# Kernel optimization log

Hardware: AMD Instinct MI355X
Metric: run time of the kernel (lower is better)

## Reference

```python
import jax, jax.numpy as jnp
import numpy as np

NTOKENS = 8192
TOPK = 2
HIDDEN = 4096
NUM_GROUPS = 2
M_FULL = NTOKENS * TOPK


def setup_inputs() -> dict:
    key = jax.random.key(0)
    k1, k2 = jax.random.split(key)
    gemm_buffer = jax.random.normal(k1, (NUM_GROUPS, M_FULL, HIDDEN), dtype=jnp.float32)
    scatter_index = jax.random.randint(k2, (NTOKENS, TOPK), 0, M_FULL, dtype=jnp.int64)
    return {"gemm_buffer": gemm_buffer, "scatter_index": scatter_index}


def reference(gemm_buffer, scatter_index):
    # gemm_buffer: [G, M_full, N] partial GEMM outputs (G = num_groups)
    # scatter_index: [T, K] row indices into the permuted expert GEMM output
    # Per kernel: out[t] = sum_g sum_k gemm_buffer[g, scatter_index[t, k], :],
    # accumulated in fp32 then cast back to the buffer dtype.
    gathered = gemm_buffer[:, scatter_index, :]          # [G, T, K, N]
    out = gathered.astype(jnp.float32).sum(axis=(0, 2))  # [T, N]
    return out.astype(gemm_buffer.dtype)
```

## Files before the change

### kernel.cpp

```cpp
#include <hip/hip_runtime.h>

#define NTOKENS    8192
#define TOPK       2
#define HIDDEN     4096
#define NUM_GROUPS 2
#define M_FULL     (NTOKENS * TOPK)
#define H4         (HIDDEN / 4)
#define TPB        256
#define NBLOCKS    2048
#define CHUNK      (H4 / TPB)

typedef float f32x4 __attribute__((ext_vector_type(4)));

__global__ __launch_bounds__(TPB) void topk_gather_rs_kernel(
    const f32x4* __restrict__ buf,
    const int*   __restrict__ idx,
    f32x4*       __restrict__ out)
{
    const int tid = threadIdx.x;
    const size_t g1off = (size_t)M_FULL * H4;

    int t = blockIdx.x;
    int r0 = idx[t * TOPK + 0];
    int r1 = idx[t * TOPK + 1];

    while (t < NTOKENS) {
        const int nt = t + NBLOCKS;
        int nr0 = 0, nr1 = 0;
        if (nt < NTOKENS) {
            nr0 = idx[nt * TOPK + 0];
            nr1 = idx[nt * TOPK + 1];
        }

        const f32x4* __restrict__ p00 = buf + (size_t)r0 * H4;
        const f32x4* __restrict__ p01 = buf + (size_t)r1 * H4;
        const f32x4* __restrict__ p10 = buf + g1off + (size_t)r0 * H4;
        const f32x4* __restrict__ p11 = buf + g1off + (size_t)r1 * H4;
        f32x4* __restrict__ o = out + (size_t)t * H4;

        f32x4 acc[CHUNK];
#pragma unroll
        for (int j = 0; j < CHUNK; ++j) {
            acc[j] = (f32x4)(0.f);
        }

#pragma unroll
        for (int j = 0; j < CHUNK; ++j) {
            const int k0 = (j + 0) & (CHUNK - 1);
            const int k1 = (j + 1) & (CHUNK - 1);
            const int k2 = (j + 2) & (CHUNK - 1);
            const int k3 = (j + 3) & (CHUNK - 1);

            const f32x4 a = p00[k0 * TPB + tid];
            const f32x4 b = p01[k1 * TPB + tid];
            const f32x4 c = p10[k2 * TPB + tid];
            const f32x4 d = p11[k3 * TPB + tid];

            acc[k0] += a;
            acc[k1] += b;
            acc[k2] += c;
            acc[k3] += d;
        }

#pragma unroll
        for (int j = 0; j < CHUNK; ++j) {
            __builtin_nontemporal_store(acc[j], &o[j * TPB + tid]);
        }

        t  = nt;
        r0 = nr0;
        r1 = nr1;
    }
}

extern "C" void kernel_launch(void* const* d_in, const int* in_sizes, int n_in,
                              void* d_out, int out_size, void* d_ws, size_t ws_size,
                              hipStream_t stream) {
    const f32x4* buf = (const f32x4*)d_in[0];
    const int*   idx = (const int*)d_in[1];
    f32x4*       out = (f32x4*)d_out;

    topk_gather_rs_kernel<<<NBLOCKS, TPB, 0, stream>>>(buf, idx, out);
}
```

Measured before the change: 695.2 us.

## Give each wave a contiguous 1KB-per-row span and cut grid to 512 blocks

Remaps thread indexing so each wavefront covers a contiguous 256-element span of each row instead of the block striding across the row, issues all 16 loads up front, and sums pairwise. The grid drops from 2048 to 512 persistent blocks and output stores become regular instead of nontemporal. The aim is more DRAM locality per wave and fewer scheduling waves. The risks are lower occupancy to hide memory latency and output lines polluting the cache.

```diff
diff --git a/kernel.cpp b/kernel.cpp
--- a/kernel.cpp
+++ b/kernel.cpp
@@ -7,8 +7,7 @@
 #define M_FULL     (NTOKENS * TOPK)
 #define H4         (HIDDEN / 4)
 #define TPB        256
-#define NBLOCKS    2048
-#define CHUNK      (H4 / TPB)
+#define NBLOCKS    512
 
 typedef float f32x4 __attribute__((ext_vector_type(4)));
 
@@ -17,7 +16,10 @@
     const int*   __restrict__ idx,
     f32x4*       __restrict__ out)
 {
-    const int tid = threadIdx.x;
+    const int tid  = threadIdx.x;
+    const int lane = tid & 63;
+    const int wave = tid >> 6;
+    const int base = wave * 256 + lane;
     const size_t g1off = (size_t)M_FULL * H4;
 
     int t = blockIdx.x;
@@ -32,39 +34,25 @@
             nr1 = idx[nt * TOPK + 1];
         }
 
-        const f32x4* __restrict__ p00 = buf + (size_t)r0 * H4;
-        const f32x4* __restrict__ p01 = buf + (size_t)r1 * H4;
-        const f32x4* __restrict__ p10 = buf + g1off + (size_t)r0 * H4;
-        const f32x4* __restrict__ p11 = buf + g1off + (size_t)r1 * H4;
-        f32x4* __restrict__ o = out + (size_t)t * H4;
+        const f32x4* __restrict__ p00 = buf + (size_t)r0 * H4 + base;
+        const f32x4* __restrict__ p01 = buf + (size_t)r1 * H4 + base;
+        const f32x4* __restrict__ p10 = p00 + g1off;
+        const f32x4* __restrict__ p11 = p01 + g1off;
+        f32x4* __restrict__ o = out + (size_t)t * H4 + base;
 
-        f32x4 acc[CHUNK];
+        f32x4 a[4], b[4], c[4], d[4];
 #pragma unroll
-        for (int j = 0; j < CHUNK; ++j) {
-            acc[j] = (f32x4)(0.f);
-        }
+        for (int i = 0; i < 4; ++i) a[i] = p00[i * 64];
+#pragma unroll
+        for (int i = 0; i < 4; ++i) b[i] = p01[i * 64];
+#pragma unroll
+        for (int i = 0; i < 4; ++i) c[i] = p10[i * 64];
+#pragma unroll
+        for (int i = 0; i < 4; ++i) d[i] = p11[i * 64];
 
 #pragma unroll
-        for (int j = 0; j < CHUNK; ++j) {
-            const int k0 = (j + 0) & (CHUNK - 1);
-            const int k1 = (j + 1) & (CHUNK - 1);
-            const int k2 = (j + 2) & (CHUNK - 1);
-            const int k3 = (j + 3) & (CHUNK - 1);
-
-            const f32x4 a = p00[k0 * TPB + tid];
-            const f32x4 b = p01[k1 * TPB + tid];
-            const f32x4 c = p10[k2 * TPB + tid];
-            const f32x4 d = p11[k3 * TPB + tid];
-
-            acc[k0] += a;
-            acc[k1] += b;
-            acc[k2] += c;
-            acc[k3] += d;
-        }
-
-#pragma unroll
-        for (int j = 0; j < CHUNK; ++j) {
-            __builtin_nontemporal_store(acc[j], &o[j * TPB + tid]);
+        for (int i = 0; i < 4; ++i) {
+            o[i * 64] = (a[i] + b[i]) + (c[i] + d[i]);
         }
 
         t  = nt;
```

Measured after the change: 694.3 us. Within noise of the previous version (-0.1%).
